# Performance work log

Measured on AMD Instinct MI355X. Metric: run time of the kernel, lower is better.

## Reference

```python
import jax, jax.numpy as jnp
import numpy as np

B, T, C = 4, 2048, 1024
E, TOP_K, DFF = 8, 2, 4096


def setup_inputs() -> dict:
    key = jax.random.key(0)
    ks = jax.random.split(key, 8)
    scale = 0.02
    return {
        "x": jax.random.normal(ks[0], (B, T, C), dtype=jnp.float32),
        "noise": jax.random.normal(ks[1], (B, T, E), dtype=jnp.float32),
        "w_gate": jax.random.normal(ks[2], (C, E), dtype=jnp.float32) * scale,
        "b_gate": jnp.zeros((E,), dtype=jnp.float32),
        "w_noise": jax.random.normal(ks[3], (C, E), dtype=jnp.float32) * scale,
        "b_noise": jnp.zeros((E,), dtype=jnp.float32),
        "w1": jax.random.normal(ks[4], (E, C, DFF), dtype=jnp.float32) * scale,
        "b1": jnp.zeros((E, DFF), dtype=jnp.float32),
        "w2": jax.random.normal(ks[5], (E, DFF, C), dtype=jnp.float32) * scale,
        "b2": jnp.zeros((E, C), dtype=jnp.float32),
    }


def reference(x, noise, w_gate, b_gate, w_noise, b_noise, w1, b1, w2, b2):
    # Noisy top-k router
    clean_logits = jnp.einsum("btc,ce->bte", x, w_gate) + b_gate
    noise_logits = jnp.einsum("btc,ce->bte", x, w_noise) + b_noise
    logits = clean_logits + noise * jax.nn.softplus(noise_logits)  # (B,T,E)
    top_v, top_i = jax.lax.top_k(logits, TOP_K)  # (B,T,K)
    # softmax over sparse (-inf elsewhere) logits == softmax over top-k values
    # scattered back to expert slots
    w_topk = jax.nn.softmax(top_v, axis=-1)  # (B,T,K)
    weights = jnp.einsum("btk,btke->bte", w_topk, jax.nn.one_hot(top_i, E, dtype=x.dtype))

    # Dense-equivalent dispatch/combine: weights are exactly 0 for
    # non-selected experts, so weighted dense compute matches the
    # gather/scatter combine in the original module.
    out = jnp.zeros_like(x)
    n_experts = w1.shape[0]
    for e in range(n_experts):
        h = jax.nn.relu(jnp.einsum("btc,cf->btf", x, w1[e]) + b1[e])
        y = jnp.einsum("btf,fc->btc", h, w2[e]) + b2[e]
        out = out + weights[..., e:e + 1] * y
    return out
```

## Files before the change

kernel.cpp:

```cpp
#include <hip/hip_runtime.h>
#include <hip/hip_bf16.h>
#include <cmath>

#define DEVFN __device__ __forceinline__

typedef __attribute__((ext_vector_type(8))) short short8;
typedef __attribute__((ext_vector_type(4))) float f32x4;

constexpr int C_DIM   = 1024;
constexpr int E_NUM   = 8;
constexpr int DFF_DIM = 4096;
constexpr int NTOK    = 8192;
constexpr int PAD     = 256;
constexpr int MAXROWS = NTOK * 2 + E_NUM * PAD;

DEVFN unsigned short f2bf(float f) {
    __hip_bfloat16 h = __float2bfloat16(f);
    return __builtin_bit_cast(unsigned short, h);
}
DEVFN float bf2f(unsigned short u) {
    return __bfloat162float(__builtin_bit_cast(__hip_bfloat16, u));
}
DEVFN void gload_lds16(const void* g, void* lds) {
    __builtin_amdgcn_global_load_lds(
        (const __attribute__((address_space(1))) unsigned int*)g,
        (__attribute__((address_space(3))) unsigned int*)lds, 16, 0, 0);
}


__global__ void init_kernel(int* meta, int* rowtok,
                            const float* __restrict__ wg, const float* __restrict__ wn,
                            float* __restrict__ wT) {
    int gid = blockIdx.x * 256 + threadIdx.x;
    if (gid < 64) meta[gid] = 0;
    if (gid < MAXROWS) rowtok[gid] = 0;
    if (gid < 16 * C_DIM) {
        int o = gid >> 10, c = gid & 1023;
        wT[gid] = (o < 8) ? wg[c * 8 + o] : wn[c * 8 + (o - 8)];
    }
}

__global__ __launch_bounds__(256) void router_kernel(
    const float* __restrict__ x, const float* __restrict__ noise,
    const float* __restrict__ wT, const float* __restrict__ bg,
    const float* __restrict__ bn, int* meta, int2* tok_e, float2* tok_w) {
    extern __shared__ float swT[];
    int tid = threadIdx.x;
#pragma unroll
    for (int j = 0; j < 16; j++) {
        int idx = (j * 256 + tid) * 4;
        *(float4*)&swT[idx] = *(const float4*)&wT[idx];
    }
    __syncthreads();

    int tt = tid >> 3, sub = tid & 7;
    int tok = blockIdx.x * 32 + tt;
    const float* xr = x + (size_t)tok * C_DIM;

    double acc[16];
#pragma unroll
    for (int o = 0; o < 16; o++) acc[o] = 0.0;

#pragma unroll 4
    for (int i = 0; i < 32; i++) {
        int c = i * 32 + sub * 4;
        float4 xv = *(const float4*)(xr + c);
#pragma unroll
        for (int o = 0; o < 16; o++) {
            float4 wv = *(const float4*)(&swT[o * C_DIM + c]);
            acc[o] += (double)xv.x * (double)wv.x;
            acc[o] += (double)xv.y * (double)wv.y;
            acc[o] += (double)xv.z * (double)wv.z;
            acc[o] += (double)xv.w * (double)wv.w;
        }
    }
#pragma unroll
    for (int s = 1; s <= 4; s <<= 1) {
#pragma unroll
        for (int o = 0; o < 16; o++) acc[o] += __shfl_xor(acc[o], s, 64);
    }
    if (sub == 0) {
        double logit[8];
#pragma unroll
        for (int e = 0; e < 8; e++) {
            double cl = acc[e] + (double)bg[e];
            double nl = acc[8 + e] + (double)bn[e];
            double sp = (nl > 30.0) ? nl : log1p(exp(nl));
            logit[e] = cl + (double)noise[(size_t)tok * 8 + e] * sp;
        }
        int i1 = -1, i2 = -1;
        double v1 = -1e300, v2 = -1e300;
#pragma unroll
        for (int e = 0; e < 8; e++) {
            double v = logit[e];
            if (v > v1) { v2 = v1; i2 = i1; v1 = v; i1 = e; }
            else if (v > v2) { v2 = v; i2 = e; }
        }
        double d = exp(v2 - v1);
        tok_e[tok] = make_int2(i1, i2);
        tok_w[tok] = make_float2((float)(1.0 / (1.0 + d)), (float)(d / (1.0 + d)));
        atomicAdd(&meta[i1], 1);
        atomicAdd(&meta[i2], 1);
    }
}

__global__ void offsets_kernel(int* meta) {
    if (threadIdx.x == 0 && blockIdx.x == 0) {
        int off = 0;
        for (int e = 0; e < 8; e++) {
            meta[16 + e] = off;
            off += (meta[e] + PAD - 1) / PAD * PAD;
            meta[8 + e] = 0;
        }
        meta[24] = off;
    }
}

__global__ void assign_kernel(int* meta, const int2* tok_e,
                              int2* tok_pos, int* rowtok) {
    int t = blockIdx.x * 256 + threadIdx.x;
    int lane = threadIdx.x & 63;
    int2 e = tok_e[t];
    int sel[2] = {e.x, e.y};
    int pos[2];
#pragma unroll
    for (int s = 0; s < 2; s++) {
        int p = 0;
#pragma unroll
        for (int ex = 0; ex < 8; ex++) {
            unsigned long long m = __ballot(sel[s] == ex);
            if (m) {
                int leader = __ffsll((unsigned long long)m) - 1;
                int base = 0;
                if (lane == leader) base = atomicAdd(&meta[8 + ex], (int)__popcll(m));
                base = __shfl(base, leader, 64);
                if (sel[s] == ex)
                    p = meta[16 + ex] + base + (int)__popcll(m & ((1ull << lane) - 1ull));
            }
        }
        pos[s] = p;
        rowtok[p] = t;
    }
    tok_pos[t] = make_int2(pos[0], pos[1]);
}

DEVFN void transpose_body(const float* __restrict__ ine, unsigned short* __restrict__ oute,
                          int R, int S, int r0, int s0, float (*tile)[68]) {
    int tid = threadIdx.x;
    int rr = tid >> 2, cs = (tid & 3) * 16;
    const float4* src = (const float4*)(ine + (size_t)(r0 + rr) * S + s0 + cs);
#pragma unroll
    for (int q = 0; q < 4; q++) *(float4*)&tile[rr][cs + q * 4] = src[q];
    __syncthreads();
    int ss = tid >> 2, rs = (tid & 3) * 16;
    short8 v0, v1;
#pragma unroll
    for (int q = 0; q < 8; q++) v0[q] = (short)f2bf(tile[rs + q][ss]);
#pragma unroll
    for (int q = 0; q < 8; q++) v1[q] = (short)f2bf(tile[rs + 8 + q][ss]);
    unsigned short* dst = oute + (size_t)(s0 + ss) * R + r0 + rs;
    *(short8*)dst = v0;
    *(short8*)(dst + 8) = v1;
}

constexpr int NB_T1 = (DFF_DIM / 64) * (C_DIM / 64) * E_NUM;
constexpr int NB_T2 = (C_DIM / 64) * (DFF_DIM / 64) * E_NUM;
__global__ __launch_bounds__(256) void prep_kernel(
    const float* __restrict__ w1, unsigned short* __restrict__ w1b,
    const float* __restrict__ w2, unsigned short* __restrict__ w2b,
    const float* __restrict__ x, unsigned short* __restrict__ xb) {
    __shared__ float tile[64][68];
    int b = blockIdx.x;
    if (b < NB_T1) {
        int bx = b & 63, by = (b >> 6) & 15, bz = b >> 10;
        transpose_body(w1 + (size_t)bz * C_DIM * DFF_DIM,
                       w1b + (size_t)bz * C_DIM * DFF_DIM,
                       C_DIM, DFF_DIM, by * 64, bx * 64, tile);
        return;
    }
    b -= NB_T1;
    if (b < NB_T2) {
        int bx = b & 15, by = (b >> 4) & 63, bz = b >> 10;
        transpose_body(w2 + (size_t)bz * C_DIM * DFF_DIM,
                       w2b + (size_t)bz * C_DIM * DFF_DIM,
                       DFF_DIM, C_DIM, by * 64, bx * 64, tile);
        return;
    }
    b -= NB_T2;
    const float4* src = (const float4*)(x + (size_t)b * C_DIM);
    ushort4* dst = (ushort4*)(xb + (size_t)b * C_DIM);
    int i = threadIdx.x;
    float4 v = src[i];
    ushort4 o;
    o.x = f2bf(v.x); o.y = f2bf(v.y); o.z = f2bf(v.z); o.w = f2bf(v.w);
    dst[i] = o;
}

template <int KDIM, int KLEN, int NDIM, int MODE, bool INDIR>
__global__ __launch_bounds__(512, 2) void gemm8_kernel(
    const unsigned short* __restrict__ A, const unsigned short* __restrict__ Bt,
    const float* __restrict__ bias, unsigned short* __restrict__ OutH,
    unsigned short* __restrict__ OutC0, unsigned short* __restrict__ OutC1,
    const int* __restrict__ meta, const int* __restrict__ rowtok) {
    extern __shared__ char ldsraw[];

    int nwg = gridDim.x;
    int orig = blockIdx.x;
    int q = nwg >> 3, r8 = nwg & 7;
    int xcd = orig & 7, idx = orig >> 3;
    int wgid = (xcd < r8 ? xcd * (q + 1) : r8 * (q + 1) + (xcd - r8) * q) + idx;
    constexpr int NCT = NDIM / 256;
    int rowBase = (wgid / NCT) * 256;
    int colBase = (wgid % NCT) * 256;
    if (rowBase >= meta[24]) return;
    int e = 0;
#pragma unroll
    for (int i = 1; i < 8; i++)
        if (rowBase >= meta[16 + i]) e = i;
    int koff = blockIdx.z * KLEN;

    int tid = threadIdx.x;
    int wv = tid >> 6, lane = tid & 63;
    int wr = wv >> 2, wcol = wv & 3;

    const unsigned short* Bb = Bt + (size_t)e * NDIM * KDIM + (size_t)colBase * KDIM + koff;

    int rA = tid >> 3;
    int sSl = ((tid & 7) ^ (rA & 7)) * 8;
    const unsigned short* pA[4];
    if constexpr (INDIR) {
#pragma unroll
        for (int j = 0; j < 4; j++) {
            int tok = rowtok[rowBase + rA + j * 64];
            pA[j] = A + (size_t)tok * KDIM + sSl + koff;
        }
    } else {
        const unsigned short* pA0 = A + (size_t)(rowBase + rA) * KDIM + sSl + koff;
#pragma unroll
        for (int j = 0; j < 4; j++) pA[j] = pA0 + (size_t)j * 64 * KDIM;
    }
    const unsigned short* pB0 = Bb + (size_t)rA * KDIM + sSl;

#define STAGEALL(tt) { \
        char* base_ = ldsraw + (((tt) & 1) << 16); \
        size_t kadd_ = (size_t)(tt) * 64; \
        _Pragma("unroll") for (int j_ = 0; j_ < 4; j_++) { \
            gload_lds16(pA[j_] + kadd_, base_ + j_ * 8192 + wv * 1024); \
            gload_lds16(pB0 + (size_t)j_ * 64 * KDIM + kadd_, \
                        base_ + 32768 + j_ * 8192 + wv * 1024); \
        } }

    int physk0 = (lane >> 4) ^ (lane & 7);
    int kdel = ((physk0 ^ 4) - physk0) * 16;
    const char* aB0k0 = ldsraw + wr * 16384 + (lane & 15) * 128 + physk0 * 16;
    const char* aB0k1 = aB0k0 + kdel;
    const char* bB0k0 = ldsraw + 32768 + (wcol >> 1) * 16384 +
                        ((wcol & 1) * 64 + (lane & 15)) * 128 + physk0 * 16;
    const char* bB0k1 = bB0k0 + kdel;

    short8 afA[4][2], afB[4][2], bfA[2][2], bfB[2][2];
    f32x4 acc[8][4];
#pragma unroll
    for (int m = 0; m < 8; m++)
#pragma unroll
        for (int n = 0; n < 4; n++) acc[m][n] = f32x4{0.f, 0.f, 0.f, 0.f};

#define LDA(DST, K0, K1, MOFF) \
    _Pragma("unroll") for (int mm = 0; mm < 4; mm++) { \
        DST[mm][0] = *(const short8*)((K0) + ((MOFF) + mm) * 2048); \
        DST[mm][1] = *(const short8*)((K1) + ((MOFF) + mm) * 2048); }
#define LDB(DST, K0, K1, NOFF) \
    _Pragma("unroll") for (int nn = 0; nn < 2; nn++) { \
        DST[nn][0] = *(const short8*)((K0) + ((NOFF) + nn) * 2048); \
        DST[nn][1] = *(const short8*)((K1) + ((NOFF) + nn) * 2048); }
#define QUAD(AF, BF, MB, NB) \
    __builtin_amdgcn_s_setprio(1); \
    _Pragma("unroll") for (int kk = 0; kk < 2; kk++) \
    _Pragma("unroll") for (int mm = 0; mm < 4; mm++) \
    _Pragma("unroll") for (int nn = 0; nn < 2; nn++) \
        acc[(MB) + mm][(NB) + nn] = __builtin_amdgcn_mfma_f32_16x16x32_bf16( \
            AF[mm][kk], BF[nn][kk], acc[(MB) + mm][(NB) + nn], 0, 0, 0); \
    __builtin_amdgcn_s_setprio(0);
#define SB() __builtin_amdgcn_sched_barrier(0)

    constexpr int T = KLEN / 64;

    STAGEALL(0)
    SB(); asm volatile("s_waitcnt vmcnt(0)" ::: "memory"); SB();
    __builtin_amdgcn_s_barrier(); SB();

#pragma unroll 1
    for (int t = 0; t < T; ++t) {
        if (t + 1 < T) STAGEALL(t + 1)
        const char* ak0 = aB0k0 + ((t & 1) << 16);
        const char* ak1 = aB0k1 + ((t & 1) << 16);
        const char* bk0 = bB0k0 + ((t & 1) << 16);
        const char* bk1 = bB0k1 + ((t & 1) << 16);
        LDA(afA, ak0, ak1, 0)
        LDB(bfA, bk0, bk1, 0)
        LDB(bfB, bk0, bk1, 2)
        QUAD(afA, bfA, 0, 0)
        LDA(afB, ak0, ak1, 4)
        QUAD(afA, bfB, 0, 2)
        QUAD(afB, bfA, 4, 0)
        QUAD(afB, bfB, 4, 2)
        SB();
        asm volatile("s_waitcnt vmcnt(0)" ::: "memory");
        SB();
        __builtin_amdgcn_s_barrier();
        SB();
    }
#undef STAGEALL
#undef LDA
#undef LDB
#undef QUAD

    float bv[4];
    bool addBias = (MODE == 1) || (blockIdx.z == 0);
#pragma unroll
    for (int n = 0; n < 4; n++)
        bv[n] = addBias ? bias[(size_t)e * NDIM + colBase + wcol * 64 + n * 16 + (lane & 15)]
                        : 0.f;
    unsigned short* OutP = (MODE == 1) ? OutH : (blockIdx.z == 0 ? OutC0 : OutC1);

    unsigned short* lds16 = (unsigned short*)ldsraw;
#pragma unroll
    for (int m = 0; m < 8; m++) {
#pragma unroll
        for (int n = 0; n < 4; n++) {
#pragma unroll
            for (int j = 0; j < 4; j++) {
                float v = acc[m][n][j] + bv[n];
                if (MODE == 1) v = fmaxf(v, 0.f);
                int rr = wr * 128 + m * 16 + (lane >> 4) * 4 + j;
                int cc = wcol * 64 + n * 16 + (lane & 15);
                lds16[rr * 256 + (cc ^ ((rr & 7) << 4))] = f2bf(v);
            }
        }
    }
    __syncthreads();
    {
        int row = tid >> 1, half = tid & 1;
        int xr = (row & 7) << 4;
#pragma unroll
        for (int i = 0; i < 16; i++) {
            int cs = half * 128 + i * 8;
            short8 val = *(const short8*)(lds16 + row * 256 + (cs ^ xr));
            *(short8*)(OutP + (size_t)(rowBase + row) * NDIM + colBase + cs) = val;
        }
    }
}

__global__ void combine_kernel(const unsigned short* __restrict__ c0,
                               const unsigned short* __restrict__ c1,
                               const int2* __restrict__ tok_pos, const float2* __restrict__ tok_w,
                               float* __restrict__ out) {
    int t = blockIdx.x;
    int2 p = tok_pos[t];
    float2 w = tok_w[t];
    int i = threadIdx.x;
    ushort4 a0 = ((const ushort4*)(c0 + (size_t)p.x * C_DIM))[i];
    ushort4 a1 = ((const ushort4*)(c1 + (size_t)p.x * C_DIM))[i];
    ushort4 b0 = ((const ushort4*)(c0 + (size_t)p.y * C_DIM))[i];
    ushort4 b1 = ((const ushort4*)(c1 + (size_t)p.y * C_DIM))[i];
    float4 r;
    r.x = w.x * (bf2f(a0.x) + bf2f(a1.x)) + w.y * (bf2f(b0.x) + bf2f(b1.x));
    r.y = w.x * (bf2f(a0.y) + bf2f(a1.y)) + w.y * (bf2f(b0.y) + bf2f(b1.y));
    r.z = w.x * (bf2f(a0.z) + bf2f(a1.z)) + w.y * (bf2f(b0.z) + bf2f(b1.z));
    r.w = w.x * (bf2f(a0.w) + bf2f(a1.w)) + w.y * (bf2f(b0.w) + bf2f(b1.w));
    ((float4*)(out + (size_t)t * C_DIM))[i] = r;
}

extern "C" void kernel_launch(void* const* d_in, const int* in_sizes, int n_in,
                              void* d_out, int out_size, void* d_ws, size_t ws_size,
                              hipStream_t stream) {
    (void)in_sizes; (void)n_in; (void)out_size; (void)ws_size;
    const float* x       = (const float*)d_in[0];
    const float* noise   = (const float*)d_in[1];
    const float* w_gate  = (const float*)d_in[2];
    const float* b_gate  = (const float*)d_in[3];
    const float* w_noise = (const float*)d_in[4];
    const float* b_noise = (const float*)d_in[5];
    const float* w1      = (const float*)d_in[6];
    const float* b1      = (const float*)d_in[7];
    const float* w2      = (const float*)d_in[8];
    const float* b2      = (const float*)d_in[9];
    float* out = (float*)d_out;

    char* w = (char*)d_ws;
    size_t off = 0;
    int* meta = (int*)(w + off); off += 256;
    float* wT = (float*)(w + off); off += 16 * C_DIM * 4;
    int2* tok_e = (int2*)(w + off); off += (size_t)NTOK * 8;
    float2* tok_w = (float2*)(w + off); off += (size_t)NTOK * 8;
    int2* tok_pos = (int2*)(w + off); off += (size_t)NTOK * 8;
    int* rowtok = (int*)(w + off); off += (size_t)MAXROWS * 4;
    unsigned short* H = (unsigned short*)(w + off); off += (size_t)MAXROWS * DFF_DIM * 2;
    unsigned short* w2b = (unsigned short*)(w + off); off += (size_t)E_NUM * C_DIM * DFF_DIM * 2;
    unsigned short* c0 = (unsigned short*)(w + off); off += (size_t)MAXROWS * C_DIM * 2;
    unsigned short* c1 = (unsigned short*)(w + off); off += (size_t)MAXROWS * C_DIM * 2;
    unsigned short* xb = (unsigned short*)(w + off); off += (size_t)NTOK * C_DIM * 2;
    unsigned short* w1b = (unsigned short*)(w + off); off += (size_t)E_NUM * DFF_DIM * C_DIM * 2;

    init_kernel<<<(MAXROWS + 255) / 256, 256, 0, stream>>>(meta, rowtok, w_gate, w_noise, wT);

    hipFuncSetAttribute((const void*)router_kernel,
                        hipFuncAttributeMaxDynamicSharedMemorySize, 65536);
    router_kernel<<<NTOK / 32, 256, 65536, stream>>>(x, noise, wT, b_gate, b_noise,
                                                     meta, tok_e, tok_w);
    offsets_kernel<<<1, 64, 0, stream>>>(meta);
    assign_kernel<<<NTOK / 256, 256, 0, stream>>>(meta, tok_e, tok_pos, rowtok);
    prep_kernel<<<NB_T1 + NB_T2 + NTOK, 256, 0, stream>>>(w1, w1b, w2, w2b, x, xb);

    hipFuncSetAttribute((const void*)gemm8_kernel<C_DIM, C_DIM, DFF_DIM, 1, true>,
                        hipFuncAttributeMaxDynamicSharedMemorySize, 131072);
    gemm8_kernel<C_DIM, C_DIM, DFF_DIM, 1, true>
        <<<dim3((MAXROWS / 256) * (DFF_DIM / 256), 1, 1), 512, 131072, stream>>>(
            xb, w1b, b1, H, nullptr, nullptr, meta, rowtok);

    hipFuncSetAttribute((const void*)gemm8_kernel<DFF_DIM, DFF_DIM / 2, C_DIM, 2, false>,
                        hipFuncAttributeMaxDynamicSharedMemorySize, 131072);
    gemm8_kernel<DFF_DIM, DFF_DIM / 2, C_DIM, 2, false>
        <<<dim3((MAXROWS / 256) * (C_DIM / 256), 1, 2), 512, 131072, stream>>>(
            H, w2b, b2, nullptr, c0, c1, meta, nullptr);

    combine_kernel<<<NTOK, 256, 0, stream>>>(c0, c1, tok_pos, tok_w, out);
}
```

Measured before the change: 626.3 us.

## Fuse router and weight/activation prep into one kernel with chunked router LDS

Merges the router kernel and the bf16 transpose/cast prep kernel into a single launch, with router blocks first and prep blocks after. The router now stages the gate/noise weights through LDS in four 256-column chunks (16 KB) instead of loading all 64 KB at once. This cuts the LDS footprint to about 17 KB so router and prep blocks can share one launch config and run concurrently. The cost is extra syncthreads in the router loop, and the prep work now runs before assign rather than after it.

```diff
diff --git a/kernel.cpp b/kernel.cpp
--- a/kernel.cpp
+++ b/kernel.cpp
@@ -40,68 +40,124 @@
     }
 }
 
-__global__ __launch_bounds__(256) void router_kernel(
+DEVFN void transpose_body(const float* __restrict__ ine, unsigned short* __restrict__ oute,
+                          int R, int S, int r0, int s0, float* tile) {
+    int tid = threadIdx.x;
+    int rr = tid >> 2, cs = (tid & 3) * 16;
+    const float4* src = (const float4*)(ine + (size_t)(r0 + rr) * S + s0 + cs);
+#pragma unroll
+    for (int q = 0; q < 4; q++) *(float4*)&tile[rr * 68 + cs + q * 4] = src[q];
+    __syncthreads();
+    int ss = tid >> 2, rs = (tid & 3) * 16;
+    short8 v0, v1;
+#pragma unroll
+    for (int q = 0; q < 8; q++) v0[q] = (short)f2bf(tile[(rs + q) * 68 + ss]);
+#pragma unroll
+    for (int q = 0; q < 8; q++) v1[q] = (short)f2bf(tile[(rs + 8 + q) * 68 + ss]);
+    unsigned short* dst = oute + (size_t)(s0 + ss) * R + r0 + rs;
+    *(short8*)dst = v0;
+    *(short8*)(dst + 8) = v1;
+}
+
+constexpr int NB_RT = 256;
+constexpr int NB_T1 = (DFF_DIM / 64) * (C_DIM / 64) * E_NUM;
+constexpr int NB_T2 = (C_DIM / 64) * (DFF_DIM / 64) * E_NUM;
+__global__ __launch_bounds__(256) void fused_kernel(
     const float* __restrict__ x, const float* __restrict__ noise,
     const float* __restrict__ wT, const float* __restrict__ bg,
-    const float* __restrict__ bn, int* meta, int2* tok_e, float2* tok_w) {
-    extern __shared__ float swT[];
+    const float* __restrict__ bn, int* meta, int2* tok_e, float2* tok_w,
+    const float* __restrict__ w1, unsigned short* __restrict__ w1b,
+    const float* __restrict__ w2, unsigned short* __restrict__ w2b,
+    unsigned short* __restrict__ xb) {
+    extern __shared__ float lds[];
+    int b = blockIdx.x;
     int tid = threadIdx.x;
-#pragma unroll
-    for (int j = 0; j < 16; j++) {
-        int idx = (j * 256 + tid) * 4;
-        *(float4*)&swT[idx] = *(const float4*)&wT[idx];
-    }
-    __syncthreads();
-
-    int tt = tid >> 3, sub = tid & 7;
-    int tok = blockIdx.x * 32 + tt;
-    const float* xr = x + (size_t)tok * C_DIM;
-
-    double acc[16];
-#pragma unroll
-    for (int o = 0; o < 16; o++) acc[o] = 0.0;
-
+
+    if (b < NB_RT) {
+        int tt = tid >> 3, sub = tid & 7;
+        int tok = b * 32 + tt;
+        const float* xr = x + (size_t)tok * C_DIM;
+        double acc[16];
+#pragma unroll
+        for (int o = 0; o < 16; o++) acc[o] = 0.0;
+
+        for (int ci = 0; ci < 4; ci++) {
+            __syncthreads();
+#pragma unroll
+            for (int j = 0; j < 4; j++) {
+                int qd = j * 256 + tid;
+                int o = qd >> 6, cc = (qd & 63) * 4;
+                *(float4*)&lds[qd * 4] = *(const float4*)&wT[o * C_DIM + ci * 256 + cc];
+            }
+            __syncthreads();
 #pragma unroll 4
-    for (int i = 0; i < 32; i++) {
-        int c = i * 32 + sub * 4;
-        float4 xv = *(const float4*)(xr + c);
-#pragma unroll
-        for (int o = 0; o < 16; o++) {
-            float4 wv = *(const float4*)(&swT[o * C_DIM + c]);
-            acc[o] += (double)xv.x * (double)wv.x;
-            acc[o] += (double)xv.y * (double)wv.y;
-            acc[o] += (double)xv.z * (double)wv.z;
-            acc[o] += (double)xv.w * (double)wv.w;
-        }
-    }
-#pragma unroll
-    for (int s = 1; s <= 4; s <<= 1) {
-#pragma unroll
-        for (int o = 0; o < 16; o++) acc[o] += __shfl_xor(acc[o], s, 64);
-    }
-    if (sub == 0) {
-        double logit[8];
-#pragma unroll
-        for (int e = 0; e < 8; e++) {
-            double cl = acc[e] + (double)bg[e];
-            double nl = acc[8 + e] + (double)bn[e];
-            double sp = (nl > 30.0) ? nl : log1p(exp(nl));
-            logit[e] = cl + (double)noise[(size_t)tok * 8 + e] * sp;
-        }
-        int i1 = -1, i2 = -1;
-        double v1 = -1e300, v2 = -1e300;
-#pragma unroll
-        for (int e = 0; e < 8; e++) {
-            double v = logit[e];
-            if (v > v1) { v2 = v1; i2 = i1; v1 = v; i1 = e; }
-            else if (v > v2) { v2 = v; i2 = e; }
-        }
-        double d = exp(v2 - v1);
-        tok_e[tok] = make_int2(i1, i2);
-        tok_w[tok] = make_float2((float)(1.0 / (1.0 + d)), (float)(d / (1.0 + d)));
-        atomicAdd(&meta[i1], 1);
-        atomicAdd(&meta[i2], 1);
-    }
+            for (int i = 0; i < 8; i++) {
+                int cl = i * 32 + sub * 4;
+                float4 xv = *(const float4*)(xr + ci * 256 + cl);
+#pragma unroll
+                for (int o = 0; o < 16; o++) {
+                    float4 wv = *(const float4*)&lds[o * 256 + cl];
+                    acc[o] += (double)xv.x * (double)wv.x;
+                    acc[o] += (double)xv.y * (double)wv.y;
+                    acc[o] += (double)xv.z * (double)wv.z;
+                    acc[o] += (double)xv.w * (double)wv.w;
+                }
+            }
+        }
+#pragma unroll
+        for (int s = 1; s <= 4; s <<= 1) {
+#pragma unroll
+            for (int o = 0; o < 16; o++) acc[o] += __shfl_xor(acc[o], s, 64);
+        }
+        if (sub == 0) {
+            double logit[8];
+#pragma unroll
+            for (int e = 0; e < 8; e++) {
+                double cl = acc[e] + (double)bg[e];
+                double nl = acc[8 + e] + (double)bn[e];
+                double sp = (nl > 30.0) ? nl : log1p(exp(nl));
+                logit[e] = cl + (double)noise[(size_t)tok * 8 + e] * sp;
+            }
+            int i1 = -1, i2 = -1;
+            double v1 = -1e300, v2 = -1e300;
+#pragma unroll
+            for (int e = 0; e < 8; e++) {
+                double v = logit[e];
+                if (v > v1) { v2 = v1; i2 = i1; v1 = v; i1 = e; }
+                else if (v > v2) { v2 = v; i2 = e; }
+            }
+            double d = exp(v2 - v1);
+            tok_e[tok] = make_int2(i1, i2);
+            tok_w[tok] = make_float2((float)(1.0 / (1.0 + d)), (float)(d / (1.0 + d)));
+            atomicAdd(&meta[i1], 1);
+            atomicAdd(&meta[i2], 1);
+        }
+        return;
+    }
+    b -= NB_RT;
+    if (b < NB_T1) {
+        int bx = b & 63, by = (b >> 6) & 15, bz = b >> 10;
+        transpose_body(w1 + (size_t)bz * C_DIM * DFF_DIM,
+                       w1b + (size_t)bz * C_DIM * DFF_DIM,
+                       C_DIM, DFF_DIM, by * 64, bx * 64, lds);
+        return;
+    }
+    b -= NB_T1;
+    if (b < NB_T2) {
+        int bx = b & 15, by = (b >> 4) & 63, bz = b >> 10;
+        transpose_body(w2 + (size_t)bz * C_DIM * DFF_DIM,
+                       w2b + (size_t)bz * C_DIM * DFF_DIM,
+                       DFF_DIM, C_DIM, by * 64, bx * 64, lds);
+        return;
+    }
+    b -= NB_T2;
+    const float4* src = (const float4*)(x + (size_t)b * C_DIM);
+    ushort4* dst = (ushort4*)(xb + (size_t)b * C_DIM);
+    int i = tid;
+    float4 v = src[i];
+    ushort4 o;
+    o.x = f2bf(v.x); o.y = f2bf(v.y); o.z = f2bf(v.z); o.w = f2bf(v.w);
+    dst[i] = o;
 }
 
 __global__ void offsets_kernel(int* meta) {
@@ -142,58 +198,6 @@
         rowtok[p] = t;
     }
     tok_pos[t] = make_int2(pos[0], pos[1]);
-}
-
-DEVFN void transpose_body(const float* __restrict__ ine, unsigned short* __restrict__ oute,
-                          int R, int S, int r0, int s0, float (*tile)[68]) {
-    int tid = threadIdx.x;
-    int rr = tid >> 2, cs = (tid & 3) * 16;
-    const float4* src = (const float4*)(ine + (size_t)(r0 + rr) * S + s0 + cs);
-#pragma unroll
-    for (int q = 0; q < 4; q++) *(float4*)&tile[rr][cs + q * 4] = src[q];
-    __syncthreads();
-    int ss = tid >> 2, rs = (tid & 3) * 16;
-    short8 v0, v1;
-#pragma unroll
-    for (int q = 0; q < 8; q++) v0[q] = (short)f2bf(tile[rs + q][ss]);
-#pragma unroll
-    for (int q = 0; q < 8; q++) v1[q] = (short)f2bf(tile[rs + 8 + q][ss]);
-    unsigned short* dst = oute + (size_t)(s0 + ss) * R + r0 + rs;
-    *(short8*)dst = v0;
-    *(short8*)(dst + 8) = v1;
-}
-
-constexpr int NB_T1 = (DFF_DIM / 64) * (C_DIM / 64) * E_NUM;
-constexpr int NB_T2 = (C_DIM / 64) * (DFF_DIM / 64) * E_NUM;
-__global__ __launch_bounds__(256) void prep_kernel(
-    const float* __restrict__ w1, unsigned short* __restrict__ w1b,
-    const float* __restrict__ w2, unsigned short* __restrict__ w2b,
-    const float* __restrict__ x, unsigned short* __restrict__ xb) {
-    __shared__ float tile[64][68];
-    int b = blockIdx.x;
-    if (b < NB_T1) {
-        int bx = b & 63, by = (b >> 6) & 15, bz = b >> 10;
-        transpose_body(w1 + (size_t)bz * C_DIM * DFF_DIM,
-                       w1b + (size_t)bz * C_DIM * DFF_DIM,
-                       C_DIM, DFF_DIM, by * 64, bx * 64, tile);
-        return;
-    }
-    b -= NB_T1;
-    if (b < NB_T2) {
-        int bx = b & 15, by = (b >> 4) & 63, bz = b >> 10;
-        transpose_body(w2 + (size_t)bz * C_DIM * DFF_DIM,
-                       w2b + (size_t)bz * C_DIM * DFF_DIM,
-                       DFF_DIM, C_DIM, by * 64, bx * 64, tile);
-        return;
-    }
-    b -= NB_T2;
-    const float4* src = (const float4*)(x + (size_t)b * C_DIM);
-    ushort4* dst = (ushort4*)(xb + (size_t)b * C_DIM);
-    int i = threadIdx.x;
-    float4 v = src[i];
-    ushort4 o;
-    o.x = f2bf(v.x); o.y = f2bf(v.y); o.z = f2bf(v.z); o.w = f2bf(v.w);
-    dst[i] = o;
 }
 
 template <int KDIM, int KLEN, int NDIM, int MODE, bool INDIR>
@@ -404,13 +408,12 @@
 
     init_kernel<<<(MAXROWS + 255) / 256, 256, 0, stream>>>(meta, rowtok, w_gate, w_noise, wT);
 
-    hipFuncSetAttribute((const void*)router_kernel,
-                        hipFuncAttributeMaxDynamicSharedMemorySize, 65536);
-    router_kernel<<<NTOK / 32, 256, 65536, stream>>>(x, noise, wT, b_gate, b_noise,
-                                                     meta, tok_e, tok_w);
+    fused_kernel<<<NB_RT + NB_T1 + NB_T2 + NTOK, 256, 17408, stream>>>(
+        x, noise, wT, b_gate, b_noise, meta, tok_e, tok_w,
+        w1, w1b, w2, w2b, xb);
+
     offsets_kernel<<<1, 64, 0, stream>>>(meta);
     assign_kernel<<<NTOK / 256, 256, 0, stream>>>(meta, tok_e, tok_pos, rowtok);
-    prep_kernel<<<NB_T1 + NB_T2 + NTOK, 256, 0, stream>>>(w1, w1b, w2, w2b, x, xb);
 
     hipFuncSetAttribute((const void*)gemm8_kernel<C_DIM, C_DIM, DFF_DIM, 1, true>,
                         hipFuncAttributeMaxDynamicSharedMemorySize, 131072);
```

Result: faster. 589.3 us (-5.9%).
